# Kernel tuning notes

Hardware: AMD Instinct MI355X
Metric: run time of the kernel (lower is better)

The kernel has to match this reference:

```python
import jax, jax.numpy as jnp
import numpy as np

N = 100000
E = 1600000
EPS = 1e-5


def setup_inputs() -> dict:
    key = jax.random.key(0)
    ks = jax.random.split(key, 6)
    x = jax.random.normal(ks[0], (N, 128), dtype=jnp.float32)
    edge_index = jax.random.randint(ks[1], (2, E), 0, N, dtype=jnp.int64)
    # Glorot-ish scaled weights
    W1 = jax.random.normal(ks[2], (128, 128), dtype=jnp.float32) * (1.0 / np.sqrt(128))
    b1 = jnp.zeros((128,), dtype=jnp.float32)
    gamma = jnp.ones((128,), dtype=jnp.float32)
    beta = jnp.zeros((128,), dtype=jnp.float32)
    W2 = jax.random.normal(ks[3], (64, 128), dtype=jnp.float32) * (1.0 / np.sqrt(128))
    b2 = jnp.zeros((64,), dtype=jnp.float32)
    return {"x": x, "edge_index": edge_index, "W1": W1, "b1": b1,
            "gamma": gamma, "beta": beta, "W2": W2, "b2": b2}


def _gcn_conv(x, W, b, src, dst, norm, n):
    # x: [N, Fin], W: [Fout, Fin] -> h: [N, Fout]
    h = x @ W.T
    msg = h[src] * norm[:, None]               # [E+N, Fout] gather + scale
    out = jax.ops.segment_sum(msg, dst, num_segments=n)  # scatter-add
    return out + b


def reference(x, edge_index, W1, b1, gamma, beta, W2, b2):
    n = x.shape[0]
    loop = jnp.arange(n, dtype=edge_index.dtype)
    src = jnp.concatenate([edge_index[0], loop])   # self-loops appended
    dst = jnp.concatenate([edge_index[1], loop])
    # symmetric normalization D^-1/2 A D^-1/2 (degree at destination)
    deg = jax.ops.segment_sum(jnp.ones_like(dst, dtype=x.dtype), dst, num_segments=n)
    dis = jnp.where(deg > 0, jax.lax.rsqrt(deg), 0.0)
    norm = dis[src] * dis[dst]

    h = _gcn_conv(x, W1, b1, src, dst, norm, n)
    # BatchNorm1d (training mode: biased batch statistics over nodes)
    mean = jnp.mean(h, axis=0)
    var = jnp.mean((h - mean) ** 2, axis=0)
    h = (h - mean) * jax.lax.rsqrt(var + EPS) * gamma + beta
    h = jax.nn.relu(h)
    out = _gcn_conv(h, W2, b2, src, dst, norm, n)
    return out
```

## Files before the change

kernel.cpp:

```cpp
#include <hip/hip_runtime.h>


#define SHIFT 8
#define BSZ   256
#define CHUNK 4096
#define EPT   (CHUNK/256)
#define NBMAX 1024

typedef short bf16x8 __attribute__((ext_vector_type(8)));
typedef float f32x4  __attribute__((ext_vector_type(4)));

__device__ __forceinline__ unsigned short f2bf(float f) {
    unsigned int u = __float_as_uint(f);
    unsigned int r = (u + 0x7FFFu + ((u >> 16) & 1u)) >> 16;
    return (unsigned short)r;
}
__device__ __forceinline__ float bf2f(unsigned short h) {
    return __uint_as_float(((unsigned int)h) << 16);
}
__device__ __forceinline__ void split2(float a, float b, unsigned int& hi, unsigned int& lo) {
    unsigned int ua = __float_as_uint(a), ub = __float_as_uint(b);
    unsigned int ha = ua & 0xFFFF0000u,  hb = ub & 0xFFFF0000u;
    hi = (ha >> 16) | hb;
    float la = a - __uint_as_float(ha);
    float lb = b - __uint_as_float(hb);
    lo = (__float_as_uint(la) >> 16) | (__float_as_uint(lb) & 0xFFFF0000u);
}

__global__ void k_detect(const int* __restrict__ ei32, int* __restrict__ flag) {
    if (threadIdx.x == 0 && blockIdx.x == 0) {
        int o = 0;
        for (int q = 0; q < 16; ++q) o |= ei32[2 * q + 1];
        flag[0] = (o == 0) ? 1 : 0;
    }
}

__global__ __launch_bounds__(256) void k_hist(const void* __restrict__ eiv,
                                              const int* __restrict__ flag,
                                              int* __restrict__ gcnt,
                                              int E, int N, int NB) {
    __shared__ int h[NBMAX];
    int t = threadIdx.x;
    for (int u = t; u < NB; u += 256) h[u] = 0;
    __syncthreads();
    int base = blockIdx.x * CHUNK;
    int f = flag[0];
    const long long* e64 = (const long long*)eiv;
    const int*       e32 = (const int*)eiv;
#pragma unroll
    for (int r = 0; r < EPT; ++r) {
        int e = base + r * 256 + t;
        if (e < E) {
            int s, d;
            if (f) { s = (int)e64[e]; d = (int)e64[E + e]; }
            else   { s = e32[e];      d = e32[E + e]; }
            if ((unsigned)s < (unsigned)N && (unsigned)d < (unsigned)N)
                atomicAdd(&h[d >> SHIFT], 1);
        }
    }
    __syncthreads();
    for (int u = t; u < NB; u += 256) {
        int c = h[u];
        if (c) atomicAdd(&gcnt[u], c);
    }
}

__global__ void k_scan(const int* __restrict__ gcnt, int* __restrict__ gbase,
                       int* __restrict__ gcur, int NB) {
    __shared__ int sh[1024];
    int t = threadIdx.x;
    int v = (t < NB) ? gcnt[t] : 0;
    sh[t] = v;
    __syncthreads();
    for (int off = 1; off < 1024; off <<= 1) {
        int x = sh[t];
        int y = (t >= off) ? sh[t - off] : 0;
        __syncthreads();
        sh[t] = x + y;
        __syncthreads();
    }
    if (t < NB) {
        int ex = sh[t] - v;
        gbase[t] = ex;
        gcur[t]  = ex;
    }
    if (t == 0) gbase[NB] = sh[1023];
}

__global__ __launch_bounds__(256) void k_scatter(const void* __restrict__ eiv,
                                                 const int* __restrict__ flag,
                                                 int* __restrict__ gcur,
                                                 unsigned int* __restrict__ ebuf,
                                                 int E, int N, int NB) {
    __shared__ int lcnt[NBMAX];
    __shared__ int lbase[NBMAX];
    int t = threadIdx.x;
    for (int u = t; u < NB; u += 256) lcnt[u] = 0;
    __syncthreads();
    int base = blockIdx.x * CHUNK;
    int f = flag[0];
    const long long* e64 = (const long long*)eiv;
    const int*       e32 = (const int*)eiv;
    unsigned int ent[EPT];
    int bk[EPT];
    int off[EPT];
#pragma unroll
    for (int r = 0; r < EPT; ++r) {
        int e = base + r * 256 + t;
        bk[r] = -1;
        if (e < E) {
            int s, d;
            if (f) { s = (int)e64[e]; d = (int)e64[E + e]; }
            else   { s = e32[e];      d = e32[E + e]; }
            if ((unsigned)s < (unsigned)N && (unsigned)d < (unsigned)N) {
                int b = d >> SHIFT;
                bk[r]  = b;
                off[r] = atomicAdd(&lcnt[b], 1);
                ent[r] = ((unsigned int)(d & (BSZ - 1)) << 24) | (unsigned int)s;
            }
        }
    }
    __syncthreads();
    for (int u = t; u < NB; u += 256) {
        int c = lcnt[u];
        lbase[u] = c ? atomicAdd(&gcur[u], c) : 0;
    }
    __syncthreads();
#pragma unroll
    for (int r = 0; r < EPT; ++r)
        if (bk[r] >= 0) ebuf[(size_t)lbase[bk[r]] + off[r]] = ent[r];
}

__global__ __launch_bounds__(256) void k_fine(const unsigned int* __restrict__ ebuf,
                                              const int* __restrict__ gbase,
                                              int* __restrict__ cnt,
                                              float* __restrict__ dis,
                                              int* __restrict__ rowptr,
                                              int* __restrict__ elist, int N) {
    __shared__ int lc[BSZ];
    __shared__ int ls[BSZ];
    int t = threadIdx.x;
    int b = blockIdx.x;
    int start = gbase[b], end = gbase[b + 1];
    int m = end - start;
    lc[t] = 0;
    __syncthreads();
    for (int j = t; j < m; j += 256)
        atomicAdd(&lc[ebuf[start + j] >> 24], 1);
    __syncthreads();
    int v = lc[t];
    ls[t] = v;
    __syncthreads();
    for (int off = 1; off < BSZ; off <<= 1) {
        int x = ls[t];
        int y = (t >= off) ? ls[t - off] : 0;
        __syncthreads();
        ls[t] = x + y;
        __syncthreads();
    }
    int ex = ls[t] - v;
    int i = (b << SHIFT) + t;
    if (i < N) {
        cnt[i]    = v;
        dis[i]    = rsqrtf((float)v + 1.0f);
        rowptr[i] = start + ex;
    }
    lc[t] = ex;
    __syncthreads();
    for (int j = t; j < m; j += 256) {
        unsigned int e = ebuf[start + j];
        int p = atomicAdd(&lc[e >> 24], 1);
        elist[start + p] = (int)(e & 0xFFFFFFu);
    }
}

__global__ __launch_bounds__(256) void k_prepw(const float* __restrict__ W,
                                               uint4* __restrict__ Whi,
                                               uint4* __restrict__ Wlo, int NT) {
    int idx = blockIdx.x * 256 + threadIdx.x;
    if (idx >= NT * 4 * 64) return;
    int lane = idx & 63, kt = (idx >> 6) & 3, nt = idx >> 8;
    int o = nt * 16 + (lane & 15);
    int k0 = kt * 32 + (lane >> 4) * 8;
    const float* p = W + (size_t)o * 128 + k0;
    unsigned int h[4], l[4];
#pragma unroll
    for (int pr = 0; pr < 4; ++pr) split2(p[2 * pr], p[2 * pr + 1], h[pr], l[pr]);
    Whi[idx] = make_uint4(h[0], h[1], h[2], h[3]);
    Wlo[idx] = make_uint4(l[0], l[1], l[2], l[3]);
}

__global__ __launch_bounds__(256) void k_gemm1(const float* __restrict__ x,
                                               const uint4* __restrict__ Whi,
                                               const uint4* __restrict__ Wlo,
                                               const float* __restrict__ dis,
                                               unsigned short* __restrict__ h1b, int N) {
    __shared__ uint4 Ahi[1024];
    __shared__ uint4 Alo[1024];
    int t = threadIdx.x;
    int n0 = blockIdx.x * 64;
    for (int s = t; s < 1024; s += 256) {
        int lane = s & 63, kt = (s >> 6) & 3, c = s >> 8;
        int row = n0 + c * 16 + (lane & 15);
        int rr = min(row, N - 1);
        int k0 = kt * 32 + (lane >> 4) * 8;
        const float4* p = (const float4*)(x + (size_t)rr * 128 + k0);
        float4 u0 = p[0], u1 = p[1];
        unsigned int h0, h1, h2, h3, l0, l1, l2, l3;
        split2(u0.x, u0.y, h0, l0);
        split2(u0.z, u0.w, h1, l1);
        split2(u1.x, u1.y, h2, l2);
        split2(u1.z, u1.w, h3, l3);
        Ahi[s] = make_uint4(h0, h1, h2, h3);
        Alo[s] = make_uint4(l0, l1, l2, l3);
    }
    __syncthreads();
    int w = t >> 6, lane = t & 63;
    bf16x8 ah[4], al[4];
#pragma unroll
    for (int kt = 0; kt < 4; ++kt) {
        ah[kt] = ((const bf16x8*)Ahi)[(w * 4 + kt) * 64 + lane];
        al[kt] = ((const bf16x8*)Alo)[(w * 4 + kt) * 64 + lane];
    }
    f32x4 acc[8];
#pragma unroll
    for (int nt = 0; nt < 8; ++nt) {
        acc[nt] = (f32x4)(0.f);
#pragma unroll
        for (int kt = 0; kt < 4; ++kt) {
            bf16x8 bh = ((const bf16x8*)Whi)[(nt * 4 + kt) * 64 + lane];
            bf16x8 bl = ((const bf16x8*)Wlo)[(nt * 4 + kt) * 64 + lane];
            acc[nt] = __builtin_amdgcn_mfma_f32_16x16x32_bf16(ah[kt], bh, acc[nt], 0, 0, 0);
            acc[nt] = __builtin_amdgcn_mfma_f32_16x16x32_bf16(ah[kt], bl, acc[nt], 0, 0, 0);
            acc[nt] = __builtin_amdgcn_mfma_f32_16x16x32_bf16(al[kt], bh, acc[nt], 0, 0, 0);
        }
    }
    int r0 = n0 + w * 16 + (lane >> 4) * 4;
    float dv[4];
#pragma unroll
    for (int r = 0; r < 4; ++r) {
        int row = r0 + r;
        dv[r] = (row < N) ? dis[row] : 0.f;
    }
#pragma unroll
    for (int nt = 0; nt < 8; ++nt) {
        int col = nt * 16 + (lane & 15);
#pragma unroll
        for (int r = 0; r < 4; ++r) {
            int row = r0 + r;
            if (row < N) h1b[(size_t)row * 128 + col] = f2bf(dv[r] * acc[nt][r]);
        }
    }
}

__global__ __launch_bounds__(256) void k_agg1(const unsigned int* __restrict__ h1b,
                                              const float* __restrict__ dis,
                                              const int* __restrict__ rowptr,
                                              const int* __restrict__ cnt,
                                              const int* __restrict__ elist,
                                              float* __restrict__ agg1, int N) {
    int lane = threadIdx.x & 63;
    int i = blockIdx.x * 4 + (threadIdx.x >> 6);
    if (i >= N) return;
    float accx = 0.f, accy = 0.f;
    int base = rowptr[i], c = cnt[i];
    int j = 0;
    for (; j + 16 <= c; j += 16) {
        int ss[16];
#pragma unroll
        for (int r = 0; r < 16; ++r) ss[r] = elist[base + j + r];
        unsigned int vv[16];
#pragma unroll
        for (int r = 0; r < 16; ++r) vv[r] = h1b[(size_t)ss[r] * 64 + lane];
#pragma unroll
        for (int r = 0; r < 16; ++r) {
            accx += bf2f((unsigned short)(vv[r] & 0xFFFF));
            accy += bf2f((unsigned short)(vv[r] >> 16));
        }
    }
    if (j + 8 <= c) {
        int ss[8];
#pragma unroll
        for (int r = 0; r < 8; ++r) ss[r] = elist[base + j + r];
        unsigned int vv[8];
#pragma unroll
        for (int r = 0; r < 8; ++r) vv[r] = h1b[(size_t)ss[r] * 64 + lane];
#pragma unroll
        for (int r = 0; r < 8; ++r) {
            accx += bf2f((unsigned short)(vv[r] & 0xFFFF));
            accy += bf2f((unsigned short)(vv[r] >> 16));
        }
        j += 8;
    }
    for (; j < c; ++j) {
        int s = elist[base + j];
        unsigned int v = h1b[(size_t)s * 64 + lane];
        accx += bf2f((unsigned short)(v & 0xFFFF));
        accy += bf2f((unsigned short)(v >> 16));
    }
    float di = dis[i];
    unsigned int sv = h1b[(size_t)i * 64 + lane];
    float2 r;
    r.x = di * (accx + bf2f((unsigned short)(sv & 0xFFFF)));
    r.y = di * (accy + bf2f((unsigned short)(sv >> 16)));
    ((float2*)agg1)[(size_t)i * 64 + lane] = r;
}

__global__ __launch_bounds__(256) void k_bnstats(const float* __restrict__ agg1,
                                                 float* __restrict__ stats, int N) {
    int t = threadIdx.x;
    int f = t & 127, half = t >> 7;
    float s = 0.f, sq = 0.f;
    int stride = gridDim.x * 2;
    for (int r = blockIdx.x * 2 + half; r < N; r += stride) {
        float v = agg1[r * 128 + f];
        s += v; sq += v * v;
    }
    __shared__ float ls[256], lq[256];
    ls[t] = s; lq[t] = sq;
    __syncthreads();
    if (t < 128) {
        atomicAdd(&stats[f], ls[t] + ls[t + 128]);
        atomicAdd(&stats[128 + f], lq[t] + lq[t + 128]);
    }
}

__global__ void k_bnfin(float* __restrict__ stats, const float* __restrict__ gamma,
                        const float* __restrict__ beta, int N) {
    int f = threadIdx.x;
    if (f >= 128) return;
    float invN = 1.0f / (float)N;
    float mean = stats[f] * invN;
    float var = stats[128 + f] * invN - mean * mean;
    var = fmaxf(var, 0.f);
    float inv = rsqrtf(var + 1e-5f);
    float sc = gamma[f] * inv;
    stats[256 + f] = sc;
    stats[384 + f] = beta[f] - mean * sc;
}

__global__ __launch_bounds__(256) void k_gemm2(const float* __restrict__ agg1,
                                               const uint4* __restrict__ Whi,
                                               const uint4* __restrict__ Wlo,
                                               const float* __restrict__ stats,
                                               const float* __restrict__ dis,
                                               unsigned short* __restrict__ h2b, int N) {
    __shared__ uint4 Ahi[1024];
    __shared__ uint4 Alo[1024];
    int t = threadIdx.x;
    int n0 = blockIdx.x * 64;
    const float4* st = (const float4*)stats;
    for (int s = t; s < 1024; s += 256) {
        int lane = s & 63, kt = (s >> 6) & 3, c = s >> 8;
        int row = n0 + c * 16 + (lane & 15);
        int rr = min(row, N - 1);
        int k0 = kt * 32 + (lane >> 4) * 8;
        const float4* p = (const float4*)(agg1 + (size_t)rr * 128 + k0);
        float4 a0 = p[0], a1 = p[1];
        float4 c0 = st[64 + (k0 >> 2)], c1 = st[65 + (k0 >> 2)];
        float4 s0 = st[96 + (k0 >> 2)], s1 = st[97 + (k0 >> 2)];
        float v0 = fmaxf(a0.x * c0.x + s0.x, 0.f);
        float v1 = fmaxf(a0.y * c0.y + s0.y, 0.f);
        float v2 = fmaxf(a0.z * c0.z + s0.z, 0.f);
        float v3 = fmaxf(a0.w * c0.w + s0.w, 0.f);
        float v4 = fmaxf(a1.x * c1.x + s1.x, 0.f);
        float v5 = fmaxf(a1.y * c1.y + s1.y, 0.f);
        float v6 = fmaxf(a1.z * c1.z + s1.z, 0.f);
        float v7 = fmaxf(a1.w * c1.w + s1.w, 0.f);
        unsigned int h0, h1, h2, h3, l0, l1, l2, l3;
        split2(v0, v1, h0, l0);
        split2(v2, v3, h1, l1);
        split2(v4, v5, h2, l2);
        split2(v6, v7, h3, l3);
        Ahi[s] = make_uint4(h0, h1, h2, h3);
        Alo[s] = make_uint4(l0, l1, l2, l3);
    }
    __syncthreads();
    int w = t >> 6, lane = t & 63;
    bf16x8 ah[4], al[4];
#pragma unroll
    for (int kt = 0; kt < 4; ++kt) {
        ah[kt] = ((const bf16x8*)Ahi)[(w * 4 + kt) * 64 + lane];
        al[kt] = ((const bf16x8*)Alo)[(w * 4 + kt) * 64 + lane];
    }
    f32x4 acc[4];
#pragma unroll
    for (int nt = 0; nt < 4; ++nt) {
        acc[nt] = (f32x4)(0.f);
#pragma unroll
        for (int kt = 0; kt < 4; ++kt) {
            bf16x8 bh = ((const bf16x8*)Whi)[(nt * 4 + kt) * 64 + lane];
            bf16x8 bl = ((const bf16x8*)Wlo)[(nt * 4 + kt) * 64 + lane];
            acc[nt] = __builtin_amdgcn_mfma_f32_16x16x32_bf16(ah[kt], bh, acc[nt], 0, 0, 0);
            acc[nt] = __builtin_amdgcn_mfma_f32_16x16x32_bf16(ah[kt], bl, acc[nt], 0, 0, 0);
            acc[nt] = __builtin_amdgcn_mfma_f32_16x16x32_bf16(al[kt], bh, acc[nt], 0, 0, 0);
        }
    }
    int r0 = n0 + w * 16 + (lane >> 4) * 4;
    float dv[4];
#pragma unroll
    for (int r = 0; r < 4; ++r) {
        int row = r0 + r;
        dv[r] = (row < N) ? dis[row] : 0.f;
    }
#pragma unroll
    for (int nt = 0; nt < 4; ++nt) {
        int col = nt * 16 + (lane & 15);
#pragma unroll
        for (int r = 0; r < 4; ++r) {
            int row = r0 + r;
            if (row < N) h2b[(size_t)row * 64 + col] = f2bf(dv[r] * acc[nt][r]);
        }
    }
}

__global__ __launch_bounds__(256) void k_agg2(const unsigned short* __restrict__ h2b,
                                              const float* __restrict__ dis,
                                              const int* __restrict__ rowptr,
                                              const int* __restrict__ cnt,
                                              const int* __restrict__ elist,
                                              const float* __restrict__ b2,
                                              float* __restrict__ out, int N) {
    int lane = threadIdx.x & 63;
    int i = blockIdx.x * 4 + (threadIdx.x >> 6);
    if (i >= N) return;
    float acc = 0.f;
    int base = rowptr[i], c = cnt[i];
    int j = 0;
    for (; j + 16 <= c; j += 16) {
        int ss[16];
#pragma unroll
        for (int r = 0; r < 16; ++r) ss[r] = elist[base + j + r];
        unsigned short vv[16];
#pragma unroll
        for (int r = 0; r < 16; ++r) vv[r] = h2b[(size_t)ss[r] * 64 + lane];
#pragma unroll
        for (int r = 0; r < 16; ++r) acc += bf2f(vv[r]);
    }
    if (j + 8 <= c) {
        int ss[8];
#pragma unroll
        for (int r = 0; r < 8; ++r) ss[r] = elist[base + j + r];
        unsigned short vv[8];
#pragma unroll
        for (int r = 0; r < 8; ++r) vv[r] = h2b[(size_t)ss[r] * 64 + lane];
#pragma unroll
        for (int r = 0; r < 8; ++r) acc += bf2f(vv[r]);
        j += 8;
    }
    for (; j < c; ++j) {
        int s = elist[base + j];
        acc += bf2f(h2b[(size_t)s * 64 + lane]);
    }
    float di = dis[i];
    float self = bf2f(h2b[(size_t)i * 64 + lane]);
    out[(size_t)i * 64 + lane] = di * (acc + self) + b2[lane];
}

extern "C" void kernel_launch(void* const* d_in, const int* in_sizes, int n_in,
                              void* d_out, int out_size, void* d_ws, size_t ws_size,
                              hipStream_t stream) {
    const float* x     = (const float*)d_in[0];
    const void*  ei    = d_in[1];
    const float* W1    = (const float*)d_in[2];
    const float* gamma = (const float*)d_in[4];
    const float* beta  = (const float*)d_in[5];
    const float* W2    = (const float*)d_in[6];
    const float* b2    = (const float*)d_in[7];
    float* out = (float*)d_out;

    int N = in_sizes[0] / 128;
    int E = in_sizes[1] / 2;
    int NB = (N + BSZ - 1) >> SHIFT;

    size_t Na = ((size_t)N + 3) & ~(size_t)3;
    size_t Ea = ((size_t)E + 3) & ~(size_t)3;
    int*   cnt    = (int*)d_ws;
    int*   rowptr = cnt + Na;
    int*   gcnt   = rowptr + Na;
    int*   gbase  = gcnt + 1024;
    int*   gcur   = gbase + 1028;
    int*   flagA  = gcur + 1024;
    float* stats  = (float*)(flagA + 4);
    float* dis    = stats + 512;
    int*   elist  = (int*)(dis + Na);
    unsigned int* h1b = (unsigned int*)(elist + Ea);
    float* agg1   = (float*)(h1b + Na * 64);
    unsigned int* ebuf = (unsigned int*)agg1;
    uint4* Whi1   = (uint4*)(agg1 + Na * 128);
    uint4* Wlo1   = Whi1 + 2048;
    uint4* Whi2   = Wlo1 + 2048;
    uint4* Wlo2   = Whi2 + 1024;
    unsigned int* h2b = h1b;

    hipMemsetAsync(gcnt, 0, 1024 * sizeof(int), stream);
    hipMemsetAsync(stats, 0, 512 * sizeof(float), stream);

    k_detect<<<1, 64, 0, stream>>>((const int*)ei, flagA);

    int gC    = (E + CHUNK - 1) / CHUNK;
    int gG1   = (N + 63) / 64;
    int gAgg  = (N + 3) / 4;

    k_prepw<<<8, 256, 0, stream>>>(W1, Whi1, Wlo1, 8);
    k_prepw<<<4, 256, 0, stream>>>(W2, Whi2, Wlo2, 4);
    k_hist<<<gC, 256, 0, stream>>>(ei, flagA, gcnt, E, N, NB);
    k_scan<<<1, 1024, 0, stream>>>(gcnt, gbase, gcur, NB);
    k_scatter<<<gC, 256, 0, stream>>>(ei, flagA, gcur, ebuf, E, N, NB);
    k_fine<<<NB, 256, 0, stream>>>(ebuf, gbase, cnt, dis, rowptr, elist, N);
    k_gemm1<<<gG1, 256, 0, stream>>>(x, Whi1, Wlo1, dis, (unsigned short*)h1b, N);
    k_agg1<<<gAgg, 256, 0, stream>>>(h1b, dis, rowptr, cnt, elist, agg1, N);
    k_bnstats<<<500, 256, 0, stream>>>(agg1, stats, N);
    k_bnfin<<<1, 128, 0, stream>>>(stats, gamma, beta, N);
    k_gemm2<<<gG1, 256, 0, stream>>>(agg1, Whi2, Wlo2, stats, dis, (unsigned short*)h2b, N);
    k_agg2<<<gAgg, 256, 0, stream>>>((const unsigned short*)h2b, dis, rowptr, cnt, elist, b2, out, N);
}
```

Baseline: 418.4 us.

## Fuse BatchNorm statistics into aggregation and merge small setup kernels

The per-feature sum and sum-of-squares reduction moves into the first aggregation kernel. Each block reduces its four rows in shared memory and atomically adds into one of 256 partial slots, which a single finalize kernel then sums. This removes a full extra read of the 100000x128 float intermediate and one kernel launch. The edge-index dtype detection is also inlined into the histogram and scatter kernels, and the two weight-prep launches are merged into one. The cost is extra atomics, a larger partial buffer to clear, and a serial 256-slot sum in the finalize kernel.

```diff
diff --git a/kernel.cpp b/kernel.cpp
--- a/kernel.cpp
+++ b/kernel.cpp
@@ -26,17 +26,14 @@
     float lb = b - __uint_as_float(hb);
     lo = (__float_as_uint(la) >> 16) | (__float_as_uint(lb) & 0xFFFF0000u);
 }
-
-__global__ void k_detect(const int* __restrict__ ei32, int* __restrict__ flag) {
-    if (threadIdx.x == 0 && blockIdx.x == 0) {
-        int o = 0;
-        for (int q = 0; q < 16; ++q) o |= ei32[2 * q + 1];
-        flag[0] = (o == 0) ? 1 : 0;
-    }
+__device__ __forceinline__ int detect64(const int* __restrict__ p) {
+    int o = 0;
+#pragma unroll
+    for (int q = 0; q < 16; ++q) o |= p[2 * q + 1];
+    return (o == 0) ? 1 : 0;
 }
 
 __global__ __launch_bounds__(256) void k_hist(const void* __restrict__ eiv,
-                                              const int* __restrict__ flag,
                                               int* __restrict__ gcnt,
                                               int E, int N, int NB) {
     __shared__ int h[NBMAX];
@@ -44,7 +41,7 @@
     for (int u = t; u < NB; u += 256) h[u] = 0;
     __syncthreads();
     int base = blockIdx.x * CHUNK;
-    int f = flag[0];
+    int f = detect64((const int*)eiv);
     const long long* e64 = (const long long*)eiv;
     const int*       e32 = (const int*)eiv;
 #pragma unroll
@@ -88,7 +85,6 @@
 }
 
 __global__ __launch_bounds__(256) void k_scatter(const void* __restrict__ eiv,
-                                                 const int* __restrict__ flag,
                                                  int* __restrict__ gcur,
                                                  unsigned int* __restrict__ ebuf,
                                                  int E, int N, int NB) {
@@ -98,7 +94,7 @@
     for (int u = t; u < NB; u += 256) lcnt[u] = 0;
     __syncthreads();
     int base = blockIdx.x * CHUNK;
-    int f = flag[0];
+    int f = detect64((const int*)eiv);
     const long long* e64 = (const long long*)eiv;
     const int*       e32 = (const int*)eiv;
     unsigned int ent[EPT];
@@ -174,20 +170,26 @@
     }
 }
 
-__global__ __launch_bounds__(256) void k_prepw(const float* __restrict__ W,
-                                               uint4* __restrict__ Whi,
-                                               uint4* __restrict__ Wlo, int NT) {
+__global__ __launch_bounds__(256) void k_prepw(const float* __restrict__ W1,
+                                               const float* __restrict__ W2,
+                                               uint4* __restrict__ Whi1,
+                                               uint4* __restrict__ Wlo1,
+                                               uint4* __restrict__ Whi2,
+                                               uint4* __restrict__ Wlo2) {
     int idx = blockIdx.x * 256 + threadIdx.x;
-    if (idx >= NT * 4 * 64) return;
-    int lane = idx & 63, kt = (idx >> 6) & 3, nt = idx >> 8;
+    const float* W; uint4 *H, *L; int slot;
+    if (idx < 2048)      { W = W1; H = Whi1; L = Wlo1; slot = idx; }
+    else if (idx < 3072) { W = W2; H = Whi2; L = Wlo2; slot = idx - 2048; }
+    else return;
+    int lane = slot & 63, kt = (slot >> 6) & 3, nt = slot >> 8;
     int o = nt * 16 + (lane & 15);
     int k0 = kt * 32 + (lane >> 4) * 8;
     const float* p = W + (size_t)o * 128 + k0;
     unsigned int h[4], l[4];
 #pragma unroll
     for (int pr = 0; pr < 4; ++pr) split2(p[2 * pr], p[2 * pr + 1], h[pr], l[pr]);
-    Whi[idx] = make_uint4(h[0], h[1], h[2], h[3]);
-    Wlo[idx] = make_uint4(l[0], l[1], l[2], l[3]);
+    H[slot] = make_uint4(h[0], h[1], h[2], h[3]);
+    L[slot] = make_uint4(l[0], l[1], l[2], l[3]);
 }
 
 __global__ __launch_bounds__(256) void k_gemm1(const float* __restrict__ x,
@@ -258,12 +260,15 @@
                                               const int* __restrict__ rowptr,
                                               const int* __restrict__ cnt,
                                               const int* __restrict__ elist,
-                                              float* __restrict__ agg1, int N) {
-    int lane = threadIdx.x & 63;
-    int i = blockIdx.x * 4 + (threadIdx.x >> 6);
-    if (i >= N) return;
+                                              float* __restrict__ agg1,
+                                              float* __restrict__ spart, int N) {
+    int t = threadIdx.x;
+    int lane = t & 63;
+    int i = blockIdx.x * 4 + (t >> 6);
+    bool act = (i < N);
     float accx = 0.f, accy = 0.f;
-    int base = rowptr[i], c = cnt[i];
+    int base = 0, c = 0;
+    if (act) { base = rowptr[i]; c = cnt[i]; }
     int j = 0;
     for (; j + 16 <= c; j += 16) {
         int ss[16];
@@ -298,45 +303,50 @@
         accx += bf2f((unsigned short)(v & 0xFFFF));
         accy += bf2f((unsigned short)(v >> 16));
     }
-    float di = dis[i];
-    unsigned int sv = h1b[(size_t)i * 64 + lane];
-    float2 r;
-    r.x = di * (accx + bf2f((unsigned short)(sv & 0xFFFF)));
-    r.y = di * (accy + bf2f((unsigned short)(sv >> 16)));
-    ((float2*)agg1)[(size_t)i * 64 + lane] = r;
-}
-
-__global__ __launch_bounds__(256) void k_bnstats(const float* __restrict__ agg1,
-                                                 float* __restrict__ stats, int N) {
-    int t = threadIdx.x;
-    int f = t & 127, half = t >> 7;
-    float s = 0.f, sq = 0.f;
-    int stride = gridDim.x * 2;
-    for (int r = blockIdx.x * 2 + half; r < N; r += stride) {
-        float v = agg1[r * 128 + f];
-        s += v; sq += v * v;
-    }
-    __shared__ float ls[256], lq[256];
-    ls[t] = s; lq[t] = sq;
+    float rx = 0.f, ry = 0.f;
+    if (act) {
+        float di = dis[i];
+        unsigned int sv = h1b[(size_t)i * 64 + lane];
+        rx = di * (accx + bf2f((unsigned short)(sv & 0xFFFF)));
+        ry = di * (accy + bf2f((unsigned short)(sv >> 16)));
+        ((float2*)agg1)[(size_t)i * 64 + lane] = make_float2(rx, ry);
+    }
+    __shared__ float4 red[256];
+    red[t] = make_float4(rx, ry, rx * rx, ry * ry);
+    __syncthreads();
+    if (t < 64) {
+        float4 a = red[t], b = red[t + 64], cc = red[t + 128], d = red[t + 192];
+        float sx = a.x + b.x + cc.x + d.x;
+        float sy = a.y + b.y + cc.y + d.y;
+        float qx = a.z + b.z + cc.z + d.z;
+        float qy = a.w + b.w + cc.w + d.w;
+        float* sp = spart + ((size_t)(blockIdx.x & 255) << 8);
+        atomicAdd(&sp[2 * t],       sx);
+        atomicAdd(&sp[2 * t + 1],   sy);
+        atomicAdd(&sp[128 + 2 * t],     qx);
+        atomicAdd(&sp[128 + 2 * t + 1], qy);
+    }
+}
+
+__global__ void k_bnfin(const float* __restrict__ spart, float* __restrict__ stats,
+                        const float* __restrict__ gamma,
+                        const float* __restrict__ beta, int N) {
+    __shared__ float sred[256];
+    int t = threadIdx.x;
+    float s = 0.f;
+    for (int sl = 0; sl < 256; ++sl) s += spart[sl * 256 + t];
+    sred[t] = s;
     __syncthreads();
     if (t < 128) {
-        atomicAdd(&stats[f], ls[t] + ls[t + 128]);
-        atomicAdd(&stats[128 + f], lq[t] + lq[t + 128]);
-    }
-}
-
-__global__ void k_bnfin(float* __restrict__ stats, const float* __restrict__ gamma,
-                        const float* __restrict__ beta, int N) {
-    int f = threadIdx.x;
-    if (f >= 128) return;
-    float invN = 1.0f / (float)N;
-    float mean = stats[f] * invN;
-    float var = stats[128 + f] * invN - mean * mean;
-    var = fmaxf(var, 0.f);
-    float inv = rsqrtf(var + 1e-5f);
-    float sc = gamma[f] * inv;
-    stats[256 + f] = sc;
-    stats[384 + f] = beta[f] - mean * sc;
+        float invN = 1.0f / (float)N;
+        float mean = sred[t] * invN;
+        float var = sred[128 + t] * invN - mean * mean;
+        var = fmaxf(var, 0.f);
+        float inv = rsqrtf(var + 1e-5f);
+        float sc = gamma[t] * inv;
+        stats[256 + t] = sc;
+        stats[384 + t] = beta[t] - mean * sc;
+    }
 }
 
 __global__ __launch_bounds__(256) void k_gemm2(const float* __restrict__ agg1,
@@ -480,9 +490,9 @@
     int*   gcnt   = rowptr + Na;
     int*   gbase  = gcnt + 1024;
     int*   gcur   = gbase + 1028;
-    int*   flagA  = gcur + 1024;
-    float* stats  = (float*)(flagA + 4);
-    float* dis    = stats + 512;
+    float* stats  = (float*)(gcur + 1024);
+    float* spart  = stats + 512;
+    float* dis    = spart + 65536;
     int*   elist  = (int*)(dis + Na);
     unsigned int* h1b = (unsigned int*)(elist + Ea);
     float* agg1   = (float*)(h1b + Na * 64);
@@ -494,24 +504,20 @@
     unsigned int* h2b = h1b;
 
     hipMemsetAsync(gcnt, 0, 1024 * sizeof(int), stream);
-    hipMemsetAsync(stats, 0, 512 * sizeof(float), stream);
-
-    k_detect<<<1, 64, 0, stream>>>((const int*)ei, flagA);
+    hipMemsetAsync(spart, 0, 65536 * sizeof(float), stream);
 
     int gC    = (E + CHUNK - 1) / CHUNK;
     int gG1   = (N + 63) / 64;
     int gAgg  = (N + 3) / 4;
 
-    k_prepw<<<8, 256, 0, stream>>>(W1, Whi1, Wlo1, 8);
-    k_prepw<<<4, 256, 0, stream>>>(W2, Whi2, Wlo2, 4);
-    k_hist<<<gC, 256, 0, stream>>>(ei, flagA, gcnt, E, N, NB);
+    k_prepw<<<12, 256, 0, stream>>>(W1, W2, Whi1, Wlo1, Whi2, Wlo2);
+    k_hist<<<gC, 256, 0, stream>>>(ei, gcnt, E, N, NB);
     k_scan<<<1, 1024, 0, stream>>>(gcnt, gbase, gcur, NB);
-    k_scatter<<<gC, 256, 0, stream>>>(ei, flagA, gcur, ebuf, E, N, NB);
+    k_scatter<<<gC, 256, 0, stream>>>(ei, gcur, ebuf, E, N, NB);
     k_fine<<<NB, 256, 0, stream>>>(ebuf, gbase, cnt, dis, rowptr, elist, N);
     k_gemm1<<<gG1, 256, 0, stream>>>(x, Whi1, Wlo1, dis, (unsigned short*)h1b, N);
-    k_agg1<<<gAgg, 256, 0, stream>>>(h1b, dis, rowptr, cnt, elist, agg1, N);
-    k_bnstats<<<500, 256, 0, stream>>>(agg1, stats, N);
-    k_bnfin<<<1, 128, 0, stream>>>(stats, gamma, beta, N);
+    k_agg1<<<gAgg, 256, 0, stream>>>(h1b, dis, rowptr, cnt, elist, agg1, spart, N);
+    k_bnfin<<<1, 256, 0, stream>>>(spart, stats, gamma, beta, N);
     k_gemm2<<<gG1, 256, 0, stream>>>(agg1, Whi2, Wlo2, stats, dis, (unsigned short*)h2b, N);
     k_agg2<<<gAgg, 256, 0, stream>>>((const unsigned short*)h2b, dis, rowptr, cnt, elist, b2, out, N);
 }
```

New measurement: 399.1 us. 4.6% less time.
